# Optimization experiments

Measured on AMD Instinct MI355X. Metric: run time of the kernel, lower is better.

## Reference

```python
import jax, jax.numpy as jnp
import numpy as np

B, N, D, H = 128, 256, 256, 4  # batch, atoms, feature dim (= fingerprint = input = output), heads
NEG_BIG = -1e10


def setup_inputs() -> dict:
    key = jax.random.key(0)
    ks = jax.random.split(key, 8)
    atom_neighbor_SNN = jax.random.normal(ks[0], (B, N, D), dtype=jnp.float32)
    # 0/1 adjacency (float): mask trick exp(x*-1e10)*-1e10 expects binary entries
    x_full_atom_neighbors = jax.random.randint(ks[1], (B, N, N), 0, 2).astype(jnp.float32)
    # shared neighbor_fc: Linear(D, D)
    lim = 1.0 / np.sqrt(D)
    fc_w = jax.random.uniform(ks[2], (D, D), jnp.float32, -lim, lim)
    fc_b = jnp.zeros((D,), jnp.float32)
    # per-head kernels (xavier_uniform)
    xav = np.sqrt(6.0 / (D + D))
    kernels = jax.random.uniform(ks[3], (H, D, D), jnp.float32, -xav, xav)
    # attention kernels (2D, 1) split into self/neigh halves, xavier on (2D,1)
    xav_a = np.sqrt(6.0 / (2 * D + 1))
    att_self = jax.random.uniform(ks[4], (H, D), jnp.float32, -xav_a, xav_a)
    att_neigh = jax.random.uniform(ks[5], (H, D), jnp.float32, -xav_a, xav_a)
    epsilons = jnp.full((H,), 0.6, jnp.float32)
    biases = jnp.zeros((H, D), jnp.float32)
    att_biases = jnp.zeros((H,), jnp.float32)
    return {
        "atom_neighbor_SNN": atom_neighbor_SNN,
        "x_full_atom_neighbors": x_full_atom_neighbors,
        "fc_w": fc_w, "fc_b": fc_b,
        "kernels": kernels,
        "att_self": att_self, "att_neigh": att_neigh,
        "epsilons": epsilons, "biases": biases, "att_biases": att_biases,
    }


def reference(atom_neighbor_SNN, x_full_atom_neighbors, fc_w, fc_b, kernels,
              att_self, att_neigh, epsilons, biases, att_biases):
    x = x_full_atom_neighbors                      # [B,N,N]
    atom = atom_neighbor_SNN                       # [B,N,D]
    diag = jnp.diagonal(x, axis1=-2, axis2=-1)     # [B,N]
    # new_x[h] = x + eye*diag*(eps[h]-1); so new_x[h] @ atom = x@atom + (eps[h]-1)*diag[:,:,None]*atom
    base = jnp.einsum('bnm,bmd->bnd', x, atom)     # [B,N,D]
    diagterm = diag[..., None] * atom              # [B,N,D]
    nf = base[None] + (epsilons - 1.0)[:, None, None, None] * diagterm[None]  # [H,B,N,D]
    h = jax.nn.leaky_relu(jnp.einsum('hbnd,df->hbnf', nf, fc_w) + fc_b, 0.01)  # shared fc, leaky_relu
    feat = jnp.einsum('hbnf,hfo->hbno', h, kernels) + biases[:, None, None, :]  # [H,B,N,D]
    a_s = jnp.einsum('hbno,ho->hbn', feat, att_self) + att_biases[:, None, None]
    a_n = jnp.einsum('hbno,ho->hbn', feat, att_neigh)
    att = jax.nn.elu(a_s[..., :, None] + a_n[..., None, :])  # [H,B,N,N]
    mask = jnp.exp(x * NEG_BIG) * NEG_BIG                     # 0 on edges, -1e10 off edges
    att = jax.nn.softmax(att + mask[None], axis=-1)
    # dropout: identity (eval mode)
    node = jnp.einsum('hbij,hbjo->hbio', att, feat)           # [H,B,N,D]
    out = jnp.moveaxis(node, 0, 2).reshape(node.shape[1], node.shape[2], H * node.shape[3])  # concat heads -> [B,N,H*D]
    return out, att[-1]
```

## Files before the change

### kernel.cpp

```cpp
#include <hip/hip_runtime.h>

typedef __attribute__((ext_vector_type(8))) short bf16x8;
typedef __attribute__((ext_vector_type(4))) short short4v;
typedef __attribute__((ext_vector_type(4))) float f32x4;


__device__ __forceinline__ float b2f(short s){
  unsigned u = ((unsigned)(unsigned short)s) << 16;
  return __builtin_bit_cast(float, u);
}
__device__ __forceinline__ short f2b(float f){
  unsigned u = __builtin_bit_cast(unsigned, f);
  u = (u + 0x7FFFu + ((u >> 16) & 1u)) >> 16;
  return (short)(unsigned short)u;
}

#define SWZ(row, bytecol) ((((row) * 512) + (bytecol)) ^ (((row) & 7) << 4))

__global__ __launch_bounds__(256) void ktrans(const float* __restrict__ fcw, const float* __restrict__ kers,
                                              short* __restrict__ WT, short* __restrict__ KhT){
  __shared__ float tile[32][33];
  int z = blockIdx.z;
  const float* src = (z == 0) ? fcw : (kers + (z-1)*65536);
  short* dst = (z == 0) ? WT : (KhT + (z-1)*65536);
  int x0 = blockIdx.x*32, y0 = blockIdx.y*32;
  int tx = threadIdx.x & 31, ty = threadIdx.x >> 5;
  #pragma unroll
  for (int i = 0; i < 32; i += 8) tile[ty+i][tx] = src[(y0+ty+i)*256 + x0+tx];
  __syncthreads();
  #pragma unroll
  for (int i = 0; i < 32; i += 8) dst[(x0+ty+i)*256 + y0+tx] = f2b(tile[tx][ty+i]);
}

__global__ __launch_bounds__(512, 1) void kG12(const short* __restrict__ WT, const float* __restrict__ atom,
                                               const float* __restrict__ x,
                                               short* __restrict__ G2nf, short* __restrict__ G1,
                                               unsigned* __restrict__ xbits, float* __restrict__ diag){
  __shared__ __align__(16) char G2s[65536];
  int wg = blockIdx.x;
  int xcd = wg & 7, idx = wg >> 3;
  int b  = xcd + ((idx >> 1) << 3);
  int fh = idx & 1;
  int tid = threadIdx.x, lane = tid & 63, w = tid >> 6;
  int lr = lane & 15, lq = lane >> 4, koff = lq * 8;

  {
    int wm = (w >> 1) * 64, wf = (w & 1) * 64;
    const float* Ab = atom + b*65536;
    const short* Bw = WT + (fh*128 + wf)*256;
    f32x4 acc[4][4] = {};
    for (int k0 = 0; k0 < 256; k0 += 32){
      bf16x8 af[4], bfr[4];
      #pragma unroll
      for (int i = 0; i < 4; i++){
        const float* p = Ab + (wm + i*16 + lr)*256 + k0 + koff;
        f32x4 a0 = *(const f32x4*)p, a1 = *(const f32x4*)(p + 4);
        #pragma unroll
        for (int e = 0; e < 4; e++){ af[i][e] = f2b(a0[e]); af[i][4+e] = f2b(a1[e]); }
      }
      #pragma unroll
      for (int j = 0; j < 4; j++) bfr[j] = *(const bf16x8*)(Bw + (j*16 + lr)*256 + k0 + koff);
      #pragma unroll
      for (int i = 0; i < 4; i++)
        #pragma unroll
        for (int j = 0; j < 4; j++)
          acc[i][j] = __builtin_amdgcn_mfma_f32_16x16x32_bf16(af[i], bfr[j], acc[i][j], 0, 0, 0);
    }
    #pragma unroll
    for (int i = 0; i < 4; i++)
      #pragma unroll
      for (int j = 0; j < 4; j++){
        short4v v;
        #pragma unroll
        for (int r = 0; r < 4; r++) v[r] = f2b(acc[i][j][r]);
        int fl = wf + j*16 + lr;
        int m0 = wm + i*16 + lq*4;
        *(short4v*)(G2s + SWZ(fl, m0*2)) = v;
        #pragma unroll
        for (int r = 0; r < 4; r++)
          G2nf[b*65536 + (m0 + r)*256 + fh*128 + fl] = v[r];
      }
  }
  __syncthreads();

  {
    int wf2 = (w >> 2) * 64, wn2 = (w & 3) * 64;
    const float* Xb = x + b*65536;
    f32x4 acc[4][4] = {};
    for (int k0 = 0; k0 < 256; k0 += 32){
      bf16x8 af[4], bfr[4];
      #pragma unroll
      for (int i = 0; i < 4; i++) af[i]  = *(const bf16x8*)(G2s + SWZ(wf2 + i*16 + lr, (k0 + koff)*2));
      #pragma unroll
      for (int j = 0; j < 4; j++){
        int n = wn2 + j*16 + lr;
        const float* p = Xb + n*256 + k0 + koff;
        f32x4 x0 = *(const f32x4*)p, x1 = *(const f32x4*)(p + 4);
        unsigned b8 = 0u;
        #pragma unroll
        for (int e = 0; e < 4; e++){
          bfr[j][e] = f2b(x0[e]);     if (x0[e] > 0.5f) b8 |= (1u << e);
          bfr[j][4+e] = f2b(x1[e]);   if (x1[e] > 0.5f) b8 |= (1u << (4 + e));
        }
        if (w < 4){
          unsigned full = b8 << (lq * 8);
          full |= __shfl_xor(full, 16);
          full |= __shfl_xor(full, 32);
          if (lq == 0) xbits[(b*256 + n)*8 + (k0 >> 5)] = full;
          int nm = n & 31;
          if ((n & ~31) == k0 && (nm >> 3) == lq)
            diag[b*256 + n] = (nm & 4) ? x1[nm & 3] : x0[nm & 3];
        }
      }
      #pragma unroll
      for (int i = 0; i < 4; i++)
        #pragma unroll
        for (int j = 0; j < 4; j++)
          acc[i][j] = __builtin_amdgcn_mfma_f32_16x16x32_bf16(af[i], bfr[j], acc[i][j], 0, 0, 0);
    }
    #pragma unroll
    for (int i = 0; i < 4; i++)
      #pragma unroll
      for (int j = 0; j < 4; j++){
        short4v v;
        #pragma unroll
        for (int r = 0; r < 4; r++) v[r] = f2b(acc[i][j][r]);
        *(short4v*)(G1 + b*65536 + (wn2 + j*16 + lr)*256 + fh*128 + wf2 + i*16 + lq*4) = v;
      }
  }
}

__global__ __launch_bounds__(512, 1) void kHead(const short* __restrict__ KhT, const short* __restrict__ G1,
                                                const short* __restrict__ G2nf, const float* __restrict__ diag,
                                                const float* __restrict__ fcb, const float* __restrict__ epsv,
                                                const float* __restrict__ biases, const float* __restrict__ atts,
                                                const float* __restrict__ attn, const float* __restrict__ attbv,
                                                const unsigned* __restrict__ xbits,
                                                float* __restrict__ out, float* __restrict__ out2){
  __shared__ __align__(16) char featS[131072];
  __shared__ __align__(16) char scratch[24576];
  __shared__ float asvL[256], anvL[256], fcbL[256];

  short (*h1s)[40] = (short(*)[40])scratch;
  char* Pb0 = scratch;
  char* Pb1 = scratch + 8192;
  float (*red_s)[64] = (float(*)[64])(scratch + 16384);
  float (*red_n)[64] = (float(*)[64])(scratch + 16384 + 2048);
  unsigned* xbitsL = (unsigned*)(scratch + 16384);

  int wg = blockIdx.x;
  int xcd = wg & 7, idx = wg >> 3;
  int b = xcd + ((idx >> 2) << 3);
  int h = idx & 3;
  int tid = threadIdx.x, lane = tid & 63, w = tid >> 6;
  float epsm1 = epsv[h] - 1.0f;
  const short* KA  = KhT + h*65536;
  const short* G1b = G1  + b*65536;
  const short* G2b = G2nf + b*65536;

  {
    int o = tid >> 1, half = (tid & 1) * 128;
    #pragma unroll
    for (int q = 0; q < 16; q++){
      int kk = half + q*8;
      bf16x8 v = *(const bf16x8*)(KA + o*256 + kk);
      *(bf16x8*)(featS + SWZ(o, kk*2)) = v;
    }
    if (tid < 256) fcbL[tid] = fcb[tid];
  }

  int nl = tid >> 1, rkk = (tid & 1) * 16;
  float cj = epsm1 * diag[b*256 + nl];

  int wro = (w >> 2) * 128;
  int wn  = (w & 3) * 64;
  int lr = lane & 15, lq = lane >> 4;
  int koff = lq * 8;

  bf16x8 p1a = *(const bf16x8*)(G1b + nl*256 + rkk);
  bf16x8 p1b = *(const bf16x8*)(G1b + nl*256 + rkk + 8);
  bf16x8 p2a = *(const bf16x8*)(G2b + nl*256 + rkk);
  bf16x8 p2b = *(const bf16x8*)(G2b + nl*256 + rkk + 8);

  __syncthreads();

  f32x4 acc[4][8] = {};
  for (int t = 0; t < 8; t++){
    int k0 = t*32;
    {
      bf16x8 o1, o2;
      #pragma unroll
      for (int e = 0; e < 8; e++){
        float v = b2f(p1a[e]) + cj*b2f(p2a[e]) + fcbL[k0 + rkk + e];
        v = v > 0.f ? v : 0.01f*v;
        o1[e] = f2b(v);
      }
      #pragma unroll
      for (int e = 0; e < 8; e++){
        float v = b2f(p1b[e]) + cj*b2f(p2b[e]) + fcbL[k0 + rkk + 8 + e];
        v = v > 0.f ? v : 0.01f*v;
        o2[e] = f2b(v);
      }
      *(bf16x8*)&h1s[nl][rkk] = o1;
      *(bf16x8*)&h1s[nl][rkk + 8] = o2;
    }
    __syncthreads();
    if (t < 7){
      int kn = k0 + 32;
      p1a = *(const bf16x8*)(G1b + nl*256 + kn + rkk);
      p1b = *(const bf16x8*)(G1b + nl*256 + kn + rkk + 8);
      p2a = *(const bf16x8*)(G2b + nl*256 + kn + rkk);
      p2b = *(const bf16x8*)(G2b + nl*256 + kn + rkk + 8);
    }
    bf16x8 af[4];
    #pragma unroll
    for (int j = 0; j < 4; j++) af[j] = *(const bf16x8*)&h1s[wn + j*16 + lr][koff];
    #pragma unroll
    for (int i = 0; i < 8; i++){
      bf16x8 bfv = *(const bf16x8*)(featS + SWZ(wro + i*16 + lr, (k0 + koff)*2));
      #pragma unroll
      for (int j = 0; j < 4; j++)
        acc[j][i] = __builtin_amdgcn_mfma_f32_16x16x32_bf16(af[j], bfv, acc[j][i], 0, 0, 0);
    }
    __syncthreads();
  }

  float ps[4][4] = {}, pn[4][4] = {};
  #pragma unroll
  for (int i = 0; i < 8; i++){
    int od = wro + i*16 + lr;
    float bi  = biases[h*256 + od];
    float wsv = atts[h*256 + od];
    float wnv = attn[h*256 + od];
    #pragma unroll
    for (int j = 0; j < 4; j++){
      short4v sv;
      #pragma unroll
      for (int r = 0; r < 4; r++){
        float fv = acc[j][i][r] + bi;
        sv[r] = f2b(fv);
        ps[j][r] += fv * wsv;
        pn[j][r] += fv * wnv;
      }
      *(short4v*)(featS + SWZ(od, (wn + j*16 + lq*4)*2) ) = sv;
    }
  }
  #pragma unroll
  for (int j = 0; j < 4; j++)
    #pragma unroll
    for (int r = 0; r < 4; r++){
      float s = ps[j][r], nv = pn[j][r];
      s += __shfl_xor(s, 1); s += __shfl_xor(s, 2); s += __shfl_xor(s, 4); s += __shfl_xor(s, 8);
      nv += __shfl_xor(nv, 1); nv += __shfl_xor(nv, 2); nv += __shfl_xor(nv, 4); nv += __shfl_xor(nv, 8);
      ps[j][r] = s; pn[j][r] = nv;
    }
  __syncthreads();
  if (lr == 0){
    #pragma unroll
    for (int j = 0; j < 4; j++)
      #pragma unroll
      for (int r = 0; r < 4; r++){
        red_s[w][j*16 + lq*4 + r] = ps[j][r];
        red_n[w][j*16 + lq*4 + r] = pn[j][r];
      }
  }
  __syncthreads();
  if (tid < 256){
    int q = tid >> 6, nn = tid & 63;
    asvL[tid] = red_s[q][nn] + red_s[q+4][nn] + attbv[h];
    anvL[tid] = red_n[q][nn] + red_n[q+4][nn];
  }
  __syncthreads();
  {
    const unsigned* xb = xbits + b*2048;
    #pragma unroll
    for (int q = 0; q < 4; q++) xbitsL[tid*4 + q] = xb[tid*4 + q];
  }
  __syncthreads();

  int row = tid >> 5, seg = tid & 31;
  {
    int i = row;
    float as_i = asvL[i];
    unsigned bits = xbitsL[i*8 + (seg >> 2)];
    int sh = (seg & 3) * 8;
    float Lv[8]; float mx = -3.0e38f;
    #pragma unroll
    for (int e = 0; e < 8; e++){
      float s = as_i + anvL[seg*8 + e];
      float el = s > 0.f ? s : (__expf(s) - 1.0f);
      float L = el + (((bits >> (sh + e)) & 1u) ? 0.f : -1.0e10f);
      Lv[e] = L; mx = fmaxf(mx, L);
    }
    mx = fmaxf(mx, __shfl_xor(mx, 1)); mx = fmaxf(mx, __shfl_xor(mx, 2));
    mx = fmaxf(mx, __shfl_xor(mx, 4)); mx = fmaxf(mx, __shfl_xor(mx, 8));
    mx = fmaxf(mx, __shfl_xor(mx, 16));
    float sum = 0.f;
    #pragma unroll
    for (int e = 0; e < 8; e++){ float p = __expf(Lv[e] - mx); Lv[e] = p; sum += p; }
    sum += __shfl_xor(sum, 1); sum += __shfl_xor(sum, 2); sum += __shfl_xor(sum, 4);
    sum += __shfl_xor(sum, 8); sum += __shfl_xor(sum, 16);
    float inv = 1.0f / sum;
    bf16x8 pv;
    #pragma unroll
    for (int e = 0; e < 8; e++) pv[e] = f2b(Lv[e] * inv);
    *(bf16x8*)(Pb0 + SWZ(row, seg*16)) = pv;
    if (h == 3){
      float* o2 = out2 + b*65536 + i*256 + seg*8;
      f32x4 v0, v1;
      #pragma unroll
      for (int e = 0; e < 4; e++){ v0[e] = Lv[e]*inv; v1[e] = Lv[4+e]*inv; }
      *(f32x4*)(o2) = v0; *(f32x4*)(o2 + 4) = v1;
    }
  }

  int o0w = w * 32;
  for (int t = 0; t < 16; t++){
    __syncthreads();
    int it0 = t * 16;
    char* Pr = (t & 1) ? Pb1 : Pb0;
    f32x4 a2[2] = {};
    for (int k0 = 0; k0 < 256; k0 += 32){
      bf16x8 bfp = *(const bf16x8*)(Pr + SWZ(lr, (k0 + koff)*2));
      #pragma unroll
      for (int ii = 0; ii < 2; ii++){
        bf16x8 afv = *(const bf16x8*)(featS + SWZ(o0w + ii*16 + lr, (k0 + koff)*2));
        a2[ii] = __builtin_amdgcn_mfma_f32_16x16x32_bf16(afv, bfp, a2[ii], 0, 0, 0);
      }
    }
    #pragma unroll
    for (int ii = 0; ii < 2; ii++)
      *(f32x4*)(out + (size_t)(b*256 + it0 + lr)*1024 + h*256 + o0w + ii*16 + lq*4) = a2[ii];

    if (t < 15){
      char* Pw = (t & 1) ? Pb0 : Pb1;
      int i = it0 + 16 + row;
      float as_i = asvL[i];
      unsigned bits = xbitsL[i*8 + (seg >> 2)];
      int sh = (seg & 3) * 8;
      float Lv[8]; float mx = -3.0e38f;
      #pragma unroll
      for (int e = 0; e < 8; e++){
        float s = as_i + anvL[seg*8 + e];
        float el = s > 0.f ? s : (__expf(s) - 1.0f);
        float L = el + (((bits >> (sh + e)) & 1u) ? 0.f : -1.0e10f);
        Lv[e] = L; mx = fmaxf(mx, L);
      }
      mx = fmaxf(mx, __shfl_xor(mx, 1)); mx = fmaxf(mx, __shfl_xor(mx, 2));
      mx = fmaxf(mx, __shfl_xor(mx, 4)); mx = fmaxf(mx, __shfl_xor(mx, 8));
      mx = fmaxf(mx, __shfl_xor(mx, 16));
      float sum = 0.f;
      #pragma unroll
      for (int e = 0; e < 8; e++){ float p = __expf(Lv[e] - mx); Lv[e] = p; sum += p; }
      sum += __shfl_xor(sum, 1); sum += __shfl_xor(sum, 2); sum += __shfl_xor(sum, 4);
      sum += __shfl_xor(sum, 8); sum += __shfl_xor(sum, 16);
      float inv = 1.0f / sum;
      bf16x8 pv;
      #pragma unroll
      for (int e = 0; e < 8; e++) pv[e] = f2b(Lv[e] * inv);
      *(bf16x8*)(Pw + SWZ(row, seg*16)) = pv;
      if (h == 3){
        float* o2 = out2 + b*65536 + i*256 + seg*8;
        f32x4 v0, v1;
        #pragma unroll
        for (int e = 0; e < 4; e++){ v0[e] = Lv[e]*inv; v1[e] = Lv[4+e]*inv; }
        *(f32x4*)(o2) = v0; *(f32x4*)(o2 + 4) = v1;
      }
    }
  }
}

extern "C" void kernel_launch(void* const* d_in, const int* in_sizes, int n_in,
                              void* d_out, int out_size, void* d_ws, size_t ws_size,
                              hipStream_t stream) {
  const float* atom   = (const float*)d_in[0];
  const float* x      = (const float*)d_in[1];
  const float* fc_w   = (const float*)d_in[2];
  const float* fc_b   = (const float*)d_in[3];
  const float* kers   = (const float*)d_in[4];
  const float* att_s  = (const float*)d_in[5];
  const float* att_n  = (const float*)d_in[6];
  const float* eps    = (const float*)d_in[7];
  const float* biases = (const float*)d_in[8];
  const float* att_b  = (const float*)d_in[9];

  char* w = (char*)d_ws;
  short* WT      = (short*)(w);
  short* KhT     = (short*)(w + 131072);
  float* diag    = (float*)(w + 655360);
  unsigned* xbits= (unsigned*)(w + 786432);
  short* G2nf    = (short*)(w + 1835008);
  short* G1      = (short*)(w + 18612224);

  float* out  = (float*)d_out;
  float* out2 = out + 33554432;

  ktrans<<<dim3(8, 8, 5), 256, 0, stream>>>(fc_w, kers, WT, KhT);
  kG12<<<dim3(256), 512, 0, stream>>>(WT, atom, x, G2nf, G1, xbits, diag);
  kHead<<<dim3(512), 512, 0, stream>>>(KhT, G1, G2nf, diag, fc_b, eps,
                                       biases, att_s, att_n, att_b, xbits, out, out2);
}
```

Baseline: 162.7 us.

## Keep softmax probabilities in registers as MFMA operands, drop LDS P ping-pong

Each wave now computes the softmax for its own 32 attention rows directly in the MFMA operand layout and holds the bf16 probabilities in registers. Every output tile then reuses them from registers instead of going through double-buffered P tiles in shared memory. This removes the per-tile __syncthreads and the LDS round trip. The xbits load is also merged into an earlier barrier phase. The cost is heavy register pressure: 64 floats of logits plus 16 bf16x8 operands per thread, which risks spills. The out2 writes change pattern and become more strided.

```diff
diff --git a/kernel.cpp b/kernel.cpp
--- a/kernel.cpp
+++ b/kernel.cpp
@@ -142,11 +142,9 @@
   __shared__ float asvL[256], anvL[256], fcbL[256];
 
   short (*h1s)[40] = (short(*)[40])scratch;
-  char* Pb0 = scratch;
-  char* Pb1 = scratch + 8192;
-  float (*red_s)[64] = (float(*)[64])(scratch + 16384);
-  float (*red_n)[64] = (float(*)[64])(scratch + 16384 + 2048);
-  unsigned* xbitsL = (unsigned*)(scratch + 16384);
+  float (*red_s)[64] = (float(*)[64])(scratch);
+  float (*red_n)[64] = (float(*)[64])(scratch + 2048);
+  unsigned* xbitsL = (unsigned*)(scratch + 4096);
 
   int wg = blockIdx.x;
   int xcd = wg & 7, idx = wg >> 3;
@@ -254,7 +252,6 @@
       nv += __shfl_xor(nv, 1); nv += __shfl_xor(nv, 2); nv += __shfl_xor(nv, 4); nv += __shfl_xor(nv, 8);
       ps[j][r] = s; pn[j][r] = nv;
     }
-  __syncthreads();
   if (lr == 0){
     #pragma unroll
     for (int j = 0; j < 4; j++)
@@ -263,6 +260,11 @@
         red_s[w][j*16 + lq*4 + r] = ps[j][r];
         red_n[w][j*16 + lq*4 + r] = pn[j][r];
       }
+  }
+  {
+    const unsigned* xb = xbits + b*2048;
+    #pragma unroll
+    for (int q = 0; q < 4; q++) xbitsL[tid*4 + q] = xb[tid*4 + q];
   }
   __syncthreads();
   if (tid < 256){
@@ -271,102 +273,68 @@
     anvL[tid] = red_n[q][nn] + red_n[q+4][nn];
   }
   __syncthreads();
-  {
-    const unsigned* xb = xbits + b*2048;
-    #pragma unroll
-    for (int q = 0; q < 4; q++) xbitsL[tid*4 + q] = xb[tid*4 + q];
-  }
-  __syncthreads();
-
-  int row = tid >> 5, seg = tid & 31;
-  {
-    int i = row;
+
+  int wi = w * 32;
+  bf16x8 bfp[2][8];
+  #pragma unroll
+  for (int sub = 0; sub < 2; sub++){
+    int i = wi + sub*16 + lr;
     float as_i = asvL[i];
-    unsigned bits = xbitsL[i*8 + (seg >> 2)];
-    int sh = (seg & 3) * 8;
-    float Lv[8]; float mx = -3.0e38f;
-    #pragma unroll
-    for (int e = 0; e < 8; e++){
-      float s = as_i + anvL[seg*8 + e];
-      float el = s > 0.f ? s : (__expf(s) - 1.0f);
-      float L = el + (((bits >> (sh + e)) & 1u) ? 0.f : -1.0e10f);
-      Lv[e] = L; mx = fmaxf(mx, L);
-    }
-    mx = fmaxf(mx, __shfl_xor(mx, 1)); mx = fmaxf(mx, __shfl_xor(mx, 2));
-    mx = fmaxf(mx, __shfl_xor(mx, 4)); mx = fmaxf(mx, __shfl_xor(mx, 8));
+    float Lv[8][8];
+    float mx = -3.0e38f;
+    #pragma unroll
+    for (int t = 0; t < 8; t++){
+      unsigned bits = xbitsL[i*8 + t] >> (lq*8);
+      #pragma unroll
+      for (int e = 0; e < 8; e++){
+        float s = as_i + anvL[t*32 + lq*8 + e];
+        float el = s > 0.f ? s : (__expf(s) - 1.0f);
+        float L = el + (((bits >> e) & 1u) ? 0.f : -1.0e10f);
+        Lv[t][e] = L; mx = fmaxf(mx, L);
+      }
+    }
     mx = fmaxf(mx, __shfl_xor(mx, 16));
+    mx = fmaxf(mx, __shfl_xor(mx, 32));
     float sum = 0.f;
     #pragma unroll
-    for (int e = 0; e < 8; e++){ float p = __expf(Lv[e] - mx); Lv[e] = p; sum += p; }
-    sum += __shfl_xor(sum, 1); sum += __shfl_xor(sum, 2); sum += __shfl_xor(sum, 4);
-    sum += __shfl_xor(sum, 8); sum += __shfl_xor(sum, 16);
+    for (int t = 0; t < 8; t++)
+      #pragma unroll
+      for (int e = 0; e < 8; e++){ float p = __expf(Lv[t][e] - mx); Lv[t][e] = p; sum += p; }
+    sum += __shfl_xor(sum, 16);
+    sum += __shfl_xor(sum, 32);
     float inv = 1.0f / sum;
-    bf16x8 pv;
-    #pragma unroll
-    for (int e = 0; e < 8; e++) pv[e] = f2b(Lv[e] * inv);
-    *(bf16x8*)(Pb0 + SWZ(row, seg*16)) = pv;
+    #pragma unroll
+    for (int t = 0; t < 8; t++){
+      bf16x8 pv;
+      #pragma unroll
+      for (int e = 0; e < 8; e++) pv[e] = f2b(Lv[t][e] * inv);
+      bfp[sub][t] = pv;
+    }
     if (h == 3){
-      float* o2 = out2 + b*65536 + i*256 + seg*8;
-      f32x4 v0, v1;
-      #pragma unroll
-      for (int e = 0; e < 4; e++){ v0[e] = Lv[e]*inv; v1[e] = Lv[4+e]*inv; }
-      *(f32x4*)(o2) = v0; *(f32x4*)(o2 + 4) = v1;
-    }
-  }
-
-  int o0w = w * 32;
-  for (int t = 0; t < 16; t++){
-    __syncthreads();
-    int it0 = t * 16;
-    char* Pr = (t & 1) ? Pb1 : Pb0;
+      float* o2 = out2 + b*65536 + i*256 + lq*8;
+      #pragma unroll
+      for (int t = 0; t < 8; t++){
+        f32x4 v0, v1;
+        #pragma unroll
+        for (int e = 0; e < 4; e++){ v0[e] = Lv[t][e]*inv; v1[e] = Lv[t][4+e]*inv; }
+        *(f32x4*)(o2 + t*32) = v0;
+        *(f32x4*)(o2 + t*32 + 4) = v1;
+      }
+    }
+  }
+
+  float* outb = out + (size_t)(b*256 + wi)*1024 + h*256;
+  #pragma unroll 1
+  for (int ot = 0; ot < 16; ot++){
     f32x4 a2[2] = {};
-    for (int k0 = 0; k0 < 256; k0 += 32){
-      bf16x8 bfp = *(const bf16x8*)(Pr + SWZ(lr, (k0 + koff)*2));
-      #pragma unroll
-      for (int ii = 0; ii < 2; ii++){
-        bf16x8 afv = *(const bf16x8*)(featS + SWZ(o0w + ii*16 + lr, (k0 + koff)*2));
-        a2[ii] = __builtin_amdgcn_mfma_f32_16x16x32_bf16(afv, bfp, a2[ii], 0, 0, 0);
-      }
-    }
-    #pragma unroll
-    for (int ii = 0; ii < 2; ii++)
-      *(f32x4*)(out + (size_t)(b*256 + it0 + lr)*1024 + h*256 + o0w + ii*16 + lq*4) = a2[ii];
-
-    if (t < 15){
-      char* Pw = (t & 1) ? Pb0 : Pb1;
-      int i = it0 + 16 + row;
-      float as_i = asvL[i];
-      unsigned bits = xbitsL[i*8 + (seg >> 2)];
-      int sh = (seg & 3) * 8;
-      float Lv[8]; float mx = -3.0e38f;
-      #pragma unroll
-      for (int e = 0; e < 8; e++){
-        float s = as_i + anvL[seg*8 + e];
-        float el = s > 0.f ? s : (__expf(s) - 1.0f);
-        float L = el + (((bits >> (sh + e)) & 1u) ? 0.f : -1.0e10f);
-        Lv[e] = L; mx = fmaxf(mx, L);
-      }
-      mx = fmaxf(mx, __shfl_xor(mx, 1)); mx = fmaxf(mx, __shfl_xor(mx, 2));
-      mx = fmaxf(mx, __shfl_xor(mx, 4)); mx = fmaxf(mx, __shfl_xor(mx, 8));
-      mx = fmaxf(mx, __shfl_xor(mx, 16));
-      float sum = 0.f;
-      #pragma unroll
-      for (int e = 0; e < 8; e++){ float p = __expf(Lv[e] - mx); Lv[e] = p; sum += p; }
-      sum += __shfl_xor(sum, 1); sum += __shfl_xor(sum, 2); sum += __shfl_xor(sum, 4);
-      sum += __shfl_xor(sum, 8); sum += __shfl_xor(sum, 16);
-      float inv = 1.0f / sum;
-      bf16x8 pv;
-      #pragma unroll
-      for (int e = 0; e < 8; e++) pv[e] = f2b(Lv[e] * inv);
-      *(bf16x8*)(Pw + SWZ(row, seg*16)) = pv;
-      if (h == 3){
-        float* o2 = out2 + b*65536 + i*256 + seg*8;
-        f32x4 v0, v1;
-        #pragma unroll
-        for (int e = 0; e < 4; e++){ v0[e] = Lv[e]*inv; v1[e] = Lv[4+e]*inv; }
-        *(f32x4*)(o2) = v0; *(f32x4*)(o2 + 4) = v1;
-      }
-    }
+    #pragma unroll
+    for (int t = 0; t < 8; t++){
+      bf16x8 afv = *(const bf16x8*)(featS + SWZ(ot*16 + lr, (t*32 + lq*8)*2));
+      a2[0] = __builtin_amdgcn_mfma_f32_16x16x32_bf16(afv, bfp[0][t], a2[0], 0, 0, 0);
+      a2[1] = __builtin_amdgcn_mfma_f32_16x16x32_bf16(afv, bfp[1][t], a2[1], 0, 0, 0);
+    }
+    *(f32x4*)(outb + (size_t)(lr)*1024 + ot*16 + lq*4) = a2[0];
+    *(f32x4*)(outb + (size_t)(16 + lr)*1024 + ot*16 + lq*4) = a2[1];
   }
 }
 
```

Result: faster. 145.2 us (-10.7%).
